# Kernel tuning notes

Measured on AMD Instinct MI355X. Metric: run time of the kernel, lower is better.

## Reference

```python
import jax, jax.numpy as jnp
import numpy as np

ALPHA = 0.2          # LeakyReLU negative slope
NEG_INF = -9e15      # mask fill value used by the original module

def setup_inputs() -> dict:
    key = jax.random.key(0)
    k1, k2, k3, k4 = jax.random.split(key, 4)
    B, N, F_in, F_out = 8, 2048, 64, 64
    inp = jax.random.normal(k1, (B, N, F_in), dtype=jnp.float32)
    adj = jax.random.randint(k2, (B, N, N), 0, 2, dtype=jnp.int32)
    # Parameters (kaiming-normal-ish init)
    W = jax.random.normal(k3, (F_in, F_out), dtype=jnp.float32) * np.sqrt(2.0 / F_in)
    a = jax.random.normal(k4, (2 * F_out, 1), dtype=jnp.float32) * np.sqrt(2.0 / (2 * F_out))
    return {"inp": inp, "adj": adj, "W": W, "a": a}

def reference(inp, adj, W, a):
    # h: [B, N, F_out]
    h = jnp.matmul(inp, W)
    F_out = W.shape[1]
    a1 = a[:F_out, 0]   # [F_out]
    a2 = a[F_out:, 0]   # [F_out]
    # e[b,i,j] = leakyrelu(h[b,i]·a1 + h[b,j]·a2)  -- broadcasted, avoids O(N^2*2F) concat
    f1 = h @ a1         # [B, N]
    f2 = h @ a2         # [B, N]
    e = jax.nn.leaky_relu(f1[:, :, None] + f2[:, None, :], negative_slope=ALPHA)
    scores = jnp.where(adj > 0, e, NEG_INF)
    attention = jax.nn.softmax(scores, axis=-1)  # [B, N, N]
    # dropout omitted (deterministic eval-mode reference)
    h_prime = jnp.matmul(attention, h)           # [B, N, F_out]
    return jax.nn.elu(h_prime)                   # concat=True path
```

## Files before the change

### kernel.cpp

```cpp
#include <hip/hip_runtime.h>
#include <hip/hip_bf16.h>

#define ALPHA 0.2f

constexpr int B = 8, N = 2048, F = 64;

typedef __attribute__((ext_vector_type(8))) short bf16x8;
typedef __attribute__((ext_vector_type(16))) float f32x16;

__device__ __forceinline__ float lrelu(float x) { return fmaxf(x, ALPHA * x); }

__global__ __launch_bounds__(256) void k1_project(
    const float* __restrict__ inp, const float* __restrict__ W,
    const float* __restrict__ a,
    __hip_bfloat16* __restrict__ hT, float* __restrict__ f1, float* __restrict__ f2)
{
  __shared__ float Wl[64][64];
  __shared__ float inpl[32][64];
  __shared__ float red[32][8][2];
  __shared__ __hip_bfloat16 hl[32][64];
  __shared__ float al[128];

  const int tid = threadIdx.x;
  const int g0 = blockIdx.x * 32;
  const int b = g0 / N, i0 = g0 % N;

  #pragma unroll
  for (int m = 0; m < 4; ++m) {
    int off = m * 1024 + tid * 4;
    *(float4*)((float*)Wl + off) = *(const float4*)(W + off);
  }
  #pragma unroll
  for (int m = 0; m < 2; ++m) {
    int off = m * 1024 + tid * 4;
    *(float4*)((float*)inpl + off) = *(const float4*)(inp + (size_t)g0 * F + off);
  }
  if (tid < 128) al[tid] = a[tid];
  __syncthreads();

  const int r = tid >> 3, c0 = (tid & 7) * 8;
  float acc[8];
  #pragma unroll
  for (int c = 0; c < 8; ++c) acc[c] = 0.f;
  for (int k = 0; k < 64; ++k) {
    float v = inpl[r][k];
    #pragma unroll
    for (int c = 0; c < 8; ++c) acc[c] += v * Wl[k][c0 + c];
  }
  float p1 = 0.f, p2 = 0.f;
  unsigned short hb[8] __attribute__((aligned(16)));
  #pragma unroll
  for (int c = 0; c < 8; ++c) {
    p1 += acc[c] * al[c0 + c];
    p2 += acc[c] * al[64 + c0 + c];
    __hip_bfloat16 hv = __float2bfloat16(acc[c]);
    hb[c] = *(unsigned short*)&hv;
  }
  red[r][tid & 7][0] = p1;
  red[r][tid & 7][1] = p2;
  *(uint4*)&hl[r][c0] = *(uint4*)hb;
  __syncthreads();

  if (tid < 32) {
    float s1 = 0.f, s2 = 0.f;
    #pragma unroll
    for (int m = 0; m < 8; ++m) { s1 += red[tid][m][0]; s2 += red[tid][m][1]; }
    f1[g0 + tid] = s1;
    f2[g0 + tid] = s2;
  }
  const int c = tid >> 2, r8 = (tid & 3) * 8;
  unsigned short tb[8] __attribute__((aligned(16)));
  #pragma unroll
  for (int m = 0; m < 8; ++m) tb[m] = *(unsigned short*)&hl[r8 + m][c];
  *(uint4*)(hT + ((size_t)b * F + c) * N + i0 + r8) = *(uint4*)tb;
}

__global__ __launch_bounds__(256) void k2_f2max(const float* __restrict__ f2,
                                                float* __restrict__ f2max)
{
  __shared__ float s[256];
  const int b = blockIdx.x, tid = threadIdx.x;
  float m = -1e30f;
  for (int j = tid; j < N; j += 256) m = fmaxf(m, f2[b * N + j]);
  s[tid] = m;
  __syncthreads();
  for (int w = 128; w > 0; w >>= 1) {
    if (tid < w) s[tid] = fmaxf(s[tid], s[tid + w]);
    __syncthreads();
  }
  if (tid == 0) f2max[b] = s[0];
}

__global__ __launch_bounds__(256) void k3_attn(
    const int* __restrict__ adj, const __hip_bfloat16* __restrict__ hT,
    const float* __restrict__ f1, const float* __restrict__ f2,
    const float* __restrict__ f2max, float* __restrict__ out)
{
  constexpr int RT = 32, JT = 128;
  __shared__ __hip_bfloat16 Pl[RT][JT];
  __shared__ __hip_bfloat16 hTl[F][JT];
  __shared__ float rs[RT][8];
  __shared__ float rcp[RT];
  __shared__ float redt[2][32][32];

  const int tid = threadIdx.x;
  const int lane = tid & 63, wid = tid >> 6;
  const int ct = wid >> 1, kh = wid & 1;
  const int bi = blockIdx.x;
  const int b = bi / (N / RT);
  const int i0 = (bi % (N / RT)) * RT;

  const int r = tid >> 3, jc = (tid & 7) * 16;
  const float f1r = f1[b * N + i0 + r];
  const float Mr = lrelu(f1r + f2max[b]);

  const int* adjrow = adj + ((size_t)(b * N + i0 + r)) * N + jc;
  const float* f2row = f2 + b * N + jc;
  const int hc = tid >> 2, js = (tid & 3) * 32;
  const __hip_bfloat16* hrow = hT + ((size_t)b * F + hc) * N + js;

  const int swp = (r & 7) << 3;
  const int swh = (hc & 7) << 3;

  float rowsum = 0.f;
  f32x16 acc;
  #pragma unroll
  for (int q = 0; q < 16; ++q) acc[q] = 0.f;

  for (int t = 0; t < N / JT; ++t) {
    const int j0 = t * JT;
    int4 av[4]; float4 fv[4]; uint4 hv[4];
    #pragma unroll
    for (int m = 0; m < 4; ++m) av[m] = *(const int4*)(adjrow + j0 + m * 4);
    #pragma unroll
    for (int m = 0; m < 4; ++m) fv[m] = *(const float4*)(f2row + j0 + m * 4);
    #pragma unroll
    for (int m = 0; m < 4; ++m) hv[m] = *(const uint4*)(hrow + j0 + m * 8);

    unsigned short pb[16] __attribute__((aligned(16)));
    #pragma unroll
    for (int m = 0; m < 4; ++m) {
      const int* ai = (const int*)&av[m];
      const float* fe = (const float*)&fv[m];
      #pragma unroll
      for (int e = 0; e < 4; ++e) {
        float s = lrelu(f1r + fe[e]);
        float p = (ai[e] > 0) ? __expf(s - Mr) : 0.f;
        __hip_bfloat16 pbf = __float2bfloat16(p);
        rowsum += __bfloat162float(pbf);
        pb[m * 4 + e] = *(unsigned short*)&pbf;
      }
    }
    *(uint4*)&Pl[r][jc ^ swp]       = *(uint4*)&pb[0];
    *(uint4*)&Pl[r][(jc + 8) ^ swp] = *(uint4*)&pb[8];
    #pragma unroll
    for (int m = 0; m < 4; ++m)
      *(uint4*)&hTl[hc][(js + m * 8) ^ swh] = hv[m];
    __syncthreads();

    const int arow = lane & 31;
    const int bcol = ct * 32 + (lane & 31);
    const int klo = kh * 64 + ((lane >> 5) * 8);
    #pragma unroll
    for (int s = 0; s < 4; ++s) {
      const int ak = klo + s * 16;
      bf16x8 af = *(const bf16x8*)&Pl[arow][ak ^ ((arow & 7) << 3)];
      bf16x8 bf = *(const bf16x8*)&hTl[bcol][ak ^ ((bcol & 7) << 3)];
      asm volatile("v_mfma_f32_32x32x16_bf16 %0, %1, %2, %0"
                   : "+v"(acc) : "v"(af), "v"(bf));
    }
    __syncthreads();
  }

  rs[r][tid & 7] = rowsum;
  if (kh == 1) {
    #pragma unroll
    for (int q = 0; q < 16; ++q)
      redt[ct][(q & 3) + 8 * (q >> 2) + 4 * (lane >> 5)][lane & 31] = acc[q];
  }
  __syncthreads();
  if (tid < 32) {
    float s = 0.f;
    #pragma unroll
    for (int m = 0; m < 8; ++m) s += rs[tid][m];
    rcp[tid] = 1.0f / fmaxf(s, 1e-30f);
  }
  __syncthreads();
  if (kh == 0) {
    #pragma unroll
    for (int q = 0; q < 16; ++q) {
      const int row = (q & 3) + 8 * (q >> 2) + 4 * (lane >> 5);
      float v = (acc[q] + redt[ct][row][lane & 31]) * rcp[row];
      v = v > 0.f ? v : expm1f(v);
      out[((size_t)(b * N + i0 + row)) * F + ct * 32 + (lane & 31)] = v;
    }
  }
}

extern "C" void kernel_launch(void* const* d_in, const int* in_sizes, int n_in,
                              void* d_out, int out_size, void* d_ws, size_t ws_size,
                              hipStream_t stream) {
  const float* inp = (const float*)d_in[0];
  const int*   adj = (const int*)d_in[1];
  const float* W   = (const float*)d_in[2];
  const float* a   = (const float*)d_in[3];
  float* out = (float*)d_out;

  char* ws = (char*)d_ws;
  __hip_bfloat16* hT = (__hip_bfloat16*)ws;
  float* f1  = (float*)(ws + (size_t)B * F * N * sizeof(__hip_bfloat16));
  float* f2  = f1 + (size_t)B * N;
  float* f2m = f2 + (size_t)B * N;

  hipLaunchKernelGGL(k1_project, dim3(B * N / 32), dim3(256), 0, stream, inp, W, a, hT, f1, f2);
  hipLaunchKernelGGL(k2_f2max, dim3(B), dim3(256), 0, stream, f2, f2m);
  hipLaunchKernelGGL(k3_attn, dim3(B * N / 32), dim3(256), 0, stream, adj, hT, f1, f2, f2m, out);
}
```

Baseline: 58.41 us.

## Fuse f2 max into projection and rewrite attention as register-fed 16x16 MFMA

The separate f2-max kernel is removed. Its work moves into the projection kernel through a warp max plus a sign-aware integer atomicMax/atomicMin on a buffer memset to 0xFF beforehand. The attention kernel is rewritten to use 16-row blocks, f2 staged in LDS, and each wave owning a 512-column K slice. Probabilities and hT fragments go straight into 16x16x32 MFMAs from registers with a one-step software prefetch, so there is no LDS staging and no per-tile barriers. Per-wave partial sums are then reduced through LDS. This cuts launch count and synchronization and doubles the grid size, at the cost of a memset, atomics, and more cross-wave reduction.

```diff
diff --git a/kernel.cpp b/kernel.cpp
--- a/kernel.cpp
+++ b/kernel.cpp
@@ -6,14 +6,15 @@
 constexpr int B = 8, N = 2048, F = 64;
 
 typedef __attribute__((ext_vector_type(8))) short bf16x8;
-typedef __attribute__((ext_vector_type(16))) float f32x16;
+typedef __attribute__((ext_vector_type(4))) float f32x4;
 
 __device__ __forceinline__ float lrelu(float x) { return fmaxf(x, ALPHA * x); }
 
 __global__ __launch_bounds__(256) void k1_project(
     const float* __restrict__ inp, const float* __restrict__ W,
     const float* __restrict__ a,
-    __hip_bfloat16* __restrict__ hT, float* __restrict__ f1, float* __restrict__ f2)
+    __hip_bfloat16* __restrict__ hT, float* __restrict__ f1, float* __restrict__ f2,
+    float* __restrict__ f2m)
 {
   __shared__ float Wl[64][64];
   __shared__ float inpl[32][64];
@@ -67,6 +68,13 @@
     for (int m = 0; m < 8; ++m) { s1 += red[tid][m][0]; s2 += red[tid][m][1]; }
     f1[g0 + tid] = s1;
     f2[g0 + tid] = s2;
+    float mx = s2;
+    #pragma unroll
+    for (int w = 16; w >= 1; w >>= 1) mx = fmaxf(mx, __shfl_xor(mx, w, 32));
+    if (tid == 0) {
+      if (mx >= 0.f) atomicMax((int*)&f2m[b], __float_as_int(mx));
+      else atomicMin((unsigned int*)&f2m[b], (unsigned int)__float_as_int(mx));
+    }
   }
   const int c = tid >> 2, r8 = (tid & 3) * 8;
   unsigned short tb[8] __attribute__((aligned(16)));
@@ -75,125 +83,112 @@
   *(uint4*)(hT + ((size_t)b * F + c) * N + i0 + r8) = *(uint4*)tb;
 }
 
-__global__ __launch_bounds__(256) void k2_f2max(const float* __restrict__ f2,
-                                                float* __restrict__ f2max)
-{
-  __shared__ float s[256];
-  const int b = blockIdx.x, tid = threadIdx.x;
-  float m = -1e30f;
-  for (int j = tid; j < N; j += 256) m = fmaxf(m, f2[b * N + j]);
-  s[tid] = m;
-  __syncthreads();
-  for (int w = 128; w > 0; w >>= 1) {
-    if (tid < w) s[tid] = fmaxf(s[tid], s[tid + w]);
-    __syncthreads();
-  }
-  if (tid == 0) f2max[b] = s[0];
-}
-
-__global__ __launch_bounds__(256) void k3_attn(
+__global__ __launch_bounds__(256, 4) void k3_attn(
     const int* __restrict__ adj, const __hip_bfloat16* __restrict__ hT,
     const float* __restrict__ f1, const float* __restrict__ f2,
     const float* __restrict__ f2max, float* __restrict__ out)
 {
-  constexpr int RT = 32, JT = 128;
-  __shared__ __hip_bfloat16 Pl[RT][JT];
-  __shared__ __hip_bfloat16 hTl[F][JT];
-  __shared__ float rs[RT][8];
-  __shared__ float rcp[RT];
-  __shared__ float redt[2][32][32];
-
-  const int tid = threadIdx.x;
-  const int lane = tid & 63, wid = tid >> 6;
-  const int ct = wid >> 1, kh = wid & 1;
+  __shared__ float f2l[N];
+  __shared__ float redt[4][16][66];
+  __shared__ float rs[4][16];
+  __shared__ float rcp_s[16];
+
+  const int tid = threadIdx.x, lane = tid & 63, wv = tid >> 6;
   const int bi = blockIdx.x;
-  const int b = bi / (N / RT);
-  const int i0 = (bi % (N / RT)) * RT;
-
-  const int r = tid >> 3, jc = (tid & 7) * 16;
-  const float f1r = f1[b * N + i0 + r];
+  const int b = bi >> 7;
+  const int i0 = (bi & 127) << 4;
+  const int l15 = lane & 15, kg = lane >> 4;
+
+  #pragma unroll
+  for (int m = 0; m < 2; ++m) {
+    const int idx = tid * 8 + m * 4;
+    *(float4*)&f2l[idx] = *(const float4*)(f2 + b * N + idx);
+  }
+  const float f1r = f1[b * N + i0 + l15];
   const float Mr = lrelu(f1r + f2max[b]);
-
-  const int* adjrow = adj + ((size_t)(b * N + i0 + r)) * N + jc;
-  const float* f2row = f2 + b * N + jc;
-  const int hc = tid >> 2, js = (tid & 3) * 32;
-  const __hip_bfloat16* hrow = hT + ((size_t)b * F + hc) * N + js;
-
-  const int swp = (r & 7) << 3;
-  const int swh = (hc & 7) << 3;
-
+  __syncthreads();
+
+  const int jbase = wv * 512 + kg * 8;
+  const int* adjp = adj + ((size_t)(b * N + i0 + l15)) * N + jbase;
+  const __hip_bfloat16* hp = hT + ((size_t)(b * F + l15)) * N + jbase;
+
+  f32x4 acc0 = {0.f,0.f,0.f,0.f}, acc1 = {0.f,0.f,0.f,0.f};
+  f32x4 acc2 = {0.f,0.f,0.f,0.f}, acc3 = {0.f,0.f,0.f,0.f};
   float rowsum = 0.f;
-  f32x16 acc;
-  #pragma unroll
-  for (int q = 0; q < 16; ++q) acc[q] = 0.f;
-
-  for (int t = 0; t < N / JT; ++t) {
-    const int j0 = t * JT;
-    int4 av[4]; float4 fv[4]; uint4 hv[4];
-    #pragma unroll
-    for (int m = 0; m < 4; ++m) av[m] = *(const int4*)(adjrow + j0 + m * 4);
-    #pragma unroll
-    for (int m = 0; m < 4; ++m) fv[m] = *(const float4*)(f2row + j0 + m * 4);
-    #pragma unroll
-    for (int m = 0; m < 4; ++m) hv[m] = *(const uint4*)(hrow + j0 + m * 8);
-
-    unsigned short pb[16] __attribute__((aligned(16)));
-    #pragma unroll
-    for (int m = 0; m < 4; ++m) {
-      const int* ai = (const int*)&av[m];
-      const float* fe = (const float*)&fv[m];
-      #pragma unroll
-      for (int e = 0; e < 4; ++e) {
-        float s = lrelu(f1r + fe[e]);
-        float p = (ai[e] > 0) ? __expf(s - Mr) : 0.f;
-        __hip_bfloat16 pbf = __float2bfloat16(p);
-        rowsum += __bfloat162float(pbf);
-        pb[m * 4 + e] = *(unsigned short*)&pbf;
-      }
-    }
-    *(uint4*)&Pl[r][jc ^ swp]       = *(uint4*)&pb[0];
-    *(uint4*)&Pl[r][(jc + 8) ^ swp] = *(uint4*)&pb[8];
-    #pragma unroll
-    for (int m = 0; m < 4; ++m)
-      *(uint4*)&hTl[hc][(js + m * 8) ^ swh] = hv[m];
-    __syncthreads();
-
-    const int arow = lane & 31;
-    const int bcol = ct * 32 + (lane & 31);
-    const int klo = kh * 64 + ((lane >> 5) * 8);
-    #pragma unroll
-    for (int s = 0; s < 4; ++s) {
-      const int ak = klo + s * 16;
-      bf16x8 af = *(const bf16x8*)&Pl[arow][ak ^ ((arow & 7) << 3)];
-      bf16x8 bf = *(const bf16x8*)&hTl[bcol][ak ^ ((bcol & 7) << 3)];
-      asm volatile("v_mfma_f32_32x32x16_bf16 %0, %1, %2, %0"
-                   : "+v"(acc) : "v"(af), "v"(bf));
-    }
-    __syncthreads();
-  }
-
-  rs[r][tid & 7] = rowsum;
-  if (kh == 1) {
-    #pragma unroll
-    for (int q = 0; q < 16; ++q)
-      redt[ct][(q & 3) + 8 * (q >> 2) + 4 * (lane >> 5)][lane & 31] = acc[q];
-  }
-  __syncthreads();
-  if (tid < 32) {
-    float s = 0.f;
-    #pragma unroll
-    for (int m = 0; m < 8; ++m) s += rs[tid][m];
-    rcp[tid] = 1.0f / fmaxf(s, 1e-30f);
-  }
-  __syncthreads();
-  if (kh == 0) {
-    #pragma unroll
-    for (int q = 0; q < 16; ++q) {
-      const int row = (q & 3) + 8 * (q >> 2) + 4 * (lane >> 5);
-      float v = (acc[q] + redt[ct][row][lane & 31]) * rcp[row];
-      v = v > 0.f ? v : expm1f(v);
-      out[((size_t)(b * N + i0 + row)) * F + ct * 32 + (lane & 31)] = v;
-    }
+
+  int4 a0 = *(const int4*)(adjp);
+  int4 a1 = *(const int4*)(adjp + 4);
+  uint4 h0 = *(const uint4*)(hp);
+  uint4 h1 = *(const uint4*)(hp + 16 * N);
+  uint4 h2 = *(const uint4*)(hp + 32 * N);
+  uint4 h3 = *(const uint4*)(hp + 48 * N);
+
+  #pragma unroll
+  for (int s = 0; s < 16; ++s) {
+    int4 na0, na1; uint4 nh0, nh1, nh2, nh3;
+    if (s < 15) {
+      const int off = (s + 1) * 32;
+      na0 = *(const int4*)(adjp + off);
+      na1 = *(const int4*)(adjp + off + 4);
+      nh0 = *(const uint4*)(hp + off);
+      nh1 = *(const uint4*)(hp + off + 16 * N);
+      nh2 = *(const uint4*)(hp + off + 32 * N);
+      nh3 = *(const uint4*)(hp + off + 48 * N);
+    }
+    const float4 u0 = *(const float4*)&f2l[jbase + s * 32];
+    const float4 u1 = *(const float4*)&f2l[jbase + s * 32 + 4];
+
+    unsigned short pb[8] __attribute__((aligned(16)));
+    const int* ai0 = (const int*)&a0;
+    const int* ai1 = (const int*)&a1;
+    const float* fe0 = (const float*)&u0;
+    const float* fe1 = (const float*)&u1;
+    #pragma unroll
+    for (int e = 0; e < 4; ++e) {
+      float p = (ai0[e] > 0) ? __expf(lrelu(f1r + fe0[e]) - Mr) : 0.f;
+      __hip_bfloat16 pf = __float2bfloat16(p);
+      rowsum += __bfloat162float(pf);
+      pb[e] = *(unsigned short*)&pf;
+    }
+    #pragma unroll
+    for (int e = 0; e < 4; ++e) {
+      float p = (ai1[e] > 0) ? __expf(lrelu(f1r + fe1[e]) - Mr) : 0.f;
+      __hip_bfloat16 pf = __float2bfloat16(p);
+      rowsum += __bfloat162float(pf);
+      pb[4 + e] = *(unsigned short*)&pf;
+    }
+    bf16x8 af = *(bf16x8*)pb;
+    asm volatile("s_nop 2\n\tv_mfma_f32_16x16x32_bf16 %0, %1, %2, %0" : "+v"(acc0) : "v"(af), "v"(*(bf16x8*)&h0));
+    asm volatile("s_nop 2\n\tv_mfma_f32_16x16x32_bf16 %0, %1, %2, %0" : "+v"(acc1) : "v"(af), "v"(*(bf16x8*)&h1));
+    asm volatile("s_nop 2\n\tv_mfma_f32_16x16x32_bf16 %0, %1, %2, %0" : "+v"(acc2) : "v"(af), "v"(*(bf16x8*)&h2));
+    asm volatile("s_nop 2\n\tv_mfma_f32_16x16x32_bf16 %0, %1, %2, %0" : "+v"(acc3) : "v"(af), "v"(*(bf16x8*)&h3));
+    if (s < 15) { a0 = na0; a1 = na1; h0 = nh0; h1 = nh1; h2 = nh2; h3 = nh3; }
+  }
+
+  rowsum += __shfl_xor(rowsum, 16);
+  rowsum += __shfl_xor(rowsum, 32);
+  if (lane < 16) rs[wv][lane] = rowsum;
+  #pragma unroll
+  for (int z = 0; z < 4; ++z) {
+    redt[wv][kg * 4 + z][ 0 + l15] = acc0[z];
+    redt[wv][kg * 4 + z][16 + l15] = acc1[z];
+    redt[wv][kg * 4 + z][32 + l15] = acc2[z];
+    redt[wv][kg * 4 + z][48 + l15] = acc3[z];
+  }
+  __syncthreads();
+  if (tid < 16) {
+    float s = rs[0][tid] + rs[1][tid] + rs[2][tid] + rs[3][tid];
+    rcp_s[tid] = 1.0f / fmaxf(s, 1e-30f);
+  }
+  __syncthreads();
+  const int c = tid & 63, rq = tid >> 6;
+  #pragma unroll
+  for (int z = 0; z < 4; ++z) {
+    const int row = z * 4 + rq;
+    float v = (redt[0][row][c] + redt[1][row][c] + redt[2][row][c] +
+               redt[3][row][c]) * rcp_s[row];
+    v = v > 0.f ? v : expm1f(v);
+    out[((size_t)(b * N + i0 + row)) * F + c] = v;
   }
 }
 
@@ -212,7 +207,9 @@
   float* f2  = f1 + (size_t)B * N;
   float* f2m = f2 + (size_t)B * N;
 
-  hipLaunchKernelGGL(k1_project, dim3(B * N / 32), dim3(256), 0, stream, inp, W, a, hT, f1, f2);
-  hipLaunchKernelGGL(k2_f2max, dim3(B), dim3(256), 0, stream, f2, f2m);
-  hipLaunchKernelGGL(k3_attn, dim3(B * N / 32), dim3(256), 0, stream, adj, hT, f1, f2, f2m, out);
+  hipMemsetAsync(f2m, 0xFF, B * sizeof(float), stream);
+  hipLaunchKernelGGL(k1_project, dim3(B * N / 32), dim3(256), 0, stream,
+                     inp, W, a, hT, f1, f2, f2m);
+  hipLaunchKernelGGL(k3_attn, dim3(B * N / 16), dim3(256), 0, stream,
+                     adj, hT, f1, f2, f2m, out);
 }
```

After: 97.10 us. 66.2% more time.
